# Optimization experiments

Hardware: AMD Instinct MI355X
Metric: run time of the kernel (lower is better)

The kernel has to match this reference:

```python
import jax, jax.numpy as jnp
import numpy as np

CONF_THRES = 0.25
IOU_THRES = 0.45
TOP_K = 1024          # fixed candidate pool per image (jit-friendly padded NMS)
B, N, C = 64, 25200, 16  # yolov5-face: 3*(80^2+40^2+20^2)=25200 anchors, 16 channels
IMG = 640.0


def setup_inputs() -> dict:
    key = jax.random.key(0)
    k1, k2, k3, k4, k5 = jax.random.split(key, 5)
    cxcy = jax.random.uniform(k1, (B, N, 2)) * (IMG - 32.0) + 16.0   # box centers
    wh = jax.random.uniform(k2, (B, N, 2)) * 120.0 + 8.0             # box sizes
    obj = jax.random.uniform(k3, (B, N, 1))                           # objectness
    lm = jax.random.uniform(k4, (B, N, 10)) * IMG                     # 5 landmarks
    cls = jax.random.uniform(k5, (B, N, 1))                           # face class conf
    x = jnp.concatenate([cxcy, wh, obj, lm, cls], axis=-1)            # [B, N, 16]
    return {"x": x}


def _xywh2xyxy(b):
    cx, cy, w, h = b[..., 0], b[..., 1], b[..., 2], b[..., 3]
    return jnp.stack([cx - w * 0.5, cy - h * 0.5, cx + w * 0.5, cy + h * 0.5], axis=-1)


def _pairwise_iou(boxes):
    # boxes: [K, 4] xyxy -> iou: [K, K]
    x1, y1, x2, y2 = boxes[:, 0], boxes[:, 1], boxes[:, 2], boxes[:, 3]
    area = jnp.clip(x2 - x1, 0.0) * jnp.clip(y2 - y1, 0.0)            # [K]
    ix1 = jnp.maximum(x1[:, None], x1[None, :])
    iy1 = jnp.maximum(y1[:, None], y1[None, :])
    ix2 = jnp.minimum(x2[:, None], x2[None, :])
    iy2 = jnp.minimum(y2[:, None], y2[None, :])
    inter = jnp.clip(ix2 - ix1, 0.0) * jnp.clip(iy2 - iy1, 0.0)
    union = area[:, None] + area[None, :] - inter
    return inter / (union + 1e-9)


def _nms_image(pred):
    # pred: [N, 16] = xywh, obj, 10 landmark coords, cls
    score = pred[:, 4] * pred[:, 15]                                   # obj * cls conf
    s = jnp.where(score > CONF_THRES, score, -1.0)                     # conf filter
    top_s, order = jax.lax.top_k(s, TOP_K)                             # sort desc
    valid = top_s > 0.0
    boxes = _xywh2xyxy(pred[order, :4])                                # [K, 4]
    lm = pred[order, 5:15]                                             # [K, 10]
    iou = _pairwise_iou(boxes)                                         # [K, K]
    idx = jnp.arange(TOP_K)

    def body(i, keep):
        # suppress lower-scored boxes overlapping kept box i
        sup = (iou[i] > IOU_THRES) & (idx > i) & keep[i]
        return keep & ~sup

    keep = jax.lax.fori_loop(0, TOP_K, body, valid)
    conf = jnp.where(valid, top_s, 0.0)[:, None]
    cls_id = jnp.zeros((TOP_K, 1), dtype=pred.dtype)                   # single class: face
    dets = jnp.concatenate([boxes, conf, lm, cls_id], axis=-1)         # [K, 16]
    return dets * keep[:, None].astype(dets.dtype)                     # zero suppressed rows


def reference(x):
    # x: [B, N, 16] -> padded detections [B, TOP_K, 16]
    return jax.vmap(_nms_image)(x)
```

## Files before the change

### kernel.cpp

```cpp
#include <hip/hip_runtime.h>
#include <stdint.h>

#define NBOX 25200
#define NCH  16
#define TOPK 1024
#define NTH  1024
#define NBUCK 4096
#define CAP  2048
#define K1_SLICES 16
#define K1_TH 256
#define ROWS_PER_SLICE (NBOX / K1_SLICES)
#define K1_ITERS 7
#define SEGCAP 1600

#define M45 ((double)0.45f + 0x1p-26)

#define OFF_KEYS  4096
#define OFF_BOXES (OFF_KEYS + 64 * K1_SLICES * SEGCAP * 8)
#define OFF_MASKS (OFF_BOXES + 64 * TOPK * 16)

__device__ __forceinline__ unsigned long long make_key(float p, uint32_t r) {
  return ((unsigned long long)__float_as_uint(p) << 32) |
         (unsigned long long)(0xFFFFFFFFu - r);
}

__device__ __forceinline__ uint32_t bucket_of(uint32_t bits) {
  uint32_t bk = (bits - 0x3E800001u) >> 12;
  return bk > (NBUCK - 1u) ? (NBUCK - 1u) : bk;
}

__global__ __launch_bounds__(K1_TH) void score_kernel(const float* __restrict__ x,
                                                      unsigned long long* __restrict__ keys,
                                                      uint32_t* __restrict__ cnts) {
  const int img = blockIdx.x >> 4;
  const int slice = blockIdx.x & (K1_SLICES - 1);
  const int t = threadIdx.x;
  const int lane = t & 63;
  const int wid = t >> 6;
  const float* __restrict__ xb = x + (size_t)img * NBOX * NCH;
  unsigned long long* __restrict__ kl = keys + ((size_t)img * K1_SLICES + slice) * SEGCAP;
  const int row0 = slice * ROWS_PER_SLICE;

  float p[K1_ITERS];
  uint32_t mask = 0;
#pragma unroll
  for (int j = 0; j < K1_ITERS - 1; ++j) {
    const size_t ro = (size_t)(row0 + t + j * K1_TH) * NCH;
    const float v = xb[ro + 4] * xb[ro + 15];
    if (v > 0.25f) mask |= (1u << j);
    p[j] = v;
  }
  {
    const int rr = t + (K1_ITERS - 1) * K1_TH;
    float v = 0.0f;
    if (rr < ROWS_PER_SLICE) {
      const size_t ro = (size_t)(row0 + rr) * NCH;
      v = xb[ro + 4] * xb[ro + 15];
      if (v > 0.25f) mask |= (1u << (K1_ITERS - 1));
    }
    p[K1_ITERS - 1] = v;
  }

  const int cntl = __popc(mask);
  uint32_t inc = (uint32_t)cntl;
#pragma unroll
  for (int off = 1; off < 64; off <<= 1) {
    const uint32_t o = __shfl_up(inc, off);
    if (lane >= off) inc += o;
  }
  const uint32_t wtotal = __shfl(inc, 63);

  __shared__ uint32_t s_wtot[4];
  if (lane == 63) s_wtot[wid] = wtotal;
  __syncthreads();
  uint32_t base = 0;
#pragma unroll
  for (int w = 0; w < 4; ++w) if (w < wid) base += s_wtot[w];

  uint32_t pos = base + (inc - (uint32_t)cntl);
#pragma unroll
  for (int j = 0; j < K1_ITERS; ++j) {
    if ((mask >> j) & 1u) {
      kl[pos] = make_key(p[j], (uint32_t)(row0 + t + j * K1_TH));
      ++pos;
    }
  }
  if (t == K1_TH - 1)
    cnts[img * K1_SLICES + slice] = base + wtotal;
}

__global__ __launch_bounds__(NTH, 1) void select_kernel(const float* __restrict__ x,
                                                        const unsigned long long* __restrict__ keys,
                                                        const uint32_t* __restrict__ cnts,
                                                        float* __restrict__ out,
                                                        float4* __restrict__ boxes) {
  __shared__ uint32_t s_hist[NBUCK];
  __shared__ uint32_t s_pos[NBUCK];
  __shared__ unsigned long long s_sorted[CAP];
  __shared__ unsigned long long s_final[TOPK];
  __shared__ uint32_t s_wsum[16];
  __shared__ uint32_t s_cnt16[K1_SLICES];
  __shared__ int s_cut;

  const int t = threadIdx.x;
  const int b = blockIdx.x;
  const int lane = t & 63;
  const int wid = t >> 6;
  const float* __restrict__ xb = x + (size_t)b * NBOX * NCH;
  const unsigned long long* __restrict__ kb0 = keys + (size_t)b * K1_SLICES * SEGCAP;

#pragma unroll
  for (int j = 0; j < NBUCK / NTH; ++j) s_hist[t + j * NTH] = 0u;
  s_final[t] = 0ull;
  if (t < K1_SLICES) {
    uint32_t c = cnts[b * K1_SLICES + t];
    s_cnt16[t] = (c > SEGCAP) ? SEGCAP : c;
  }
  if (t == 0) s_cut = 0;
  __syncthreads();
#pragma unroll
  for (int s = 0; s < K1_SLICES; ++s) {
    const int cs_ = (int)s_cnt16[s];
    const unsigned long long* seg = kb0 + (size_t)s * SEGCAP;
    for (int j = t; j < cs_; j += NTH)
      atomicAdd(&s_hist[bucket_of((uint32_t)(seg[j] >> 32))], 1u);
  }
  __syncthreads();

  const uint32_t h0 = s_hist[4 * t], h1 = s_hist[4 * t + 1];
  const uint32_t h2 = s_hist[4 * t + 2], h3 = s_hist[4 * t + 3];
  const uint32_t qs = h0 + h1 + h2 + h3;
  uint32_t v = qs;
#pragma unroll
  for (int off = 1; off < 64; off <<= 1) {
    const uint32_t o = __shfl_down(v, off);
    if (lane + off < 64) v += o;
  }
  if (lane == 0) s_wsum[wid] = v;
  __syncthreads();
  uint32_t tail = 0;
#pragma unroll
  for (int w = 0; w < 16; ++w) if (w > wid) tail += s_wsum[w];
  const uint32_t after = (v - qs) + tail;
  const uint32_t e3 = after, e2 = after + h3, e1 = e2 + h2, e0 = e1 + h1;
  s_pos[4 * t] = e0; s_pos[4 * t + 1] = e1;
  s_pos[4 * t + 2] = e2; s_pos[4 * t + 3] = e3;
  int cand = -1;
  if (e3 + h3 >= TOPK) cand = 4 * t + 3;
  else if (e2 + h2 >= TOPK) cand = 4 * t + 2;
  else if (e1 + h1 >= TOPK) cand = 4 * t + 1;
  else if (e0 + h0 >= TOPK) cand = 4 * t;
  int wmax = cand;
#pragma unroll
  for (int off = 32; off > 0; off >>= 1) {
    const int o = __shfl_down(wmax, off);
    if (o > wmax) wmax = o;
  }
  if (lane == 0 && wmax >= 0) atomicMax(&s_cut, wmax);
  __syncthreads();
  const int cut = s_cut;
  int M = (int)(s_pos[cut] + s_hist[cut]);
  if (M > CAP) M = CAP;
  __syncthreads();

#pragma unroll
  for (int s = 0; s < K1_SLICES; ++s) {
    const int cs_ = (int)s_cnt16[s];
    const unsigned long long* seg = kb0 + (size_t)s * SEGCAP;
    for (int j = t; j < cs_; j += NTH) {
      const unsigned long long key = seg[j];
      const uint32_t bk = bucket_of((uint32_t)(key >> 32));
      if ((int)bk >= cut) {
        const uint32_t pos = atomicAdd(&s_pos[bk], 1u);
        if (pos < CAP) s_sorted[pos] = key;
      }
    }
  }
  __syncthreads();

  for (int p = t; p < M; p += NTH) {
    const unsigned long long key = s_sorted[p];
    const uint32_t bk = bucket_of((uint32_t)(key >> 32));
    int end = (int)s_pos[bk]; if (end > M) end = M;
    int start = end - (int)s_hist[bk]; if (start < 0) start = 0;
    int lr = 0;
    for (int q = start; q < end; ++q) lr += (int)(s_sorted[q] > key);
    const int fp = start + lr;
    if (fp < TOPK) s_final[fp] = key;
  }
  __syncthreads();

  const unsigned long long mykey = s_final[t];
  const uint32_t sbits = (uint32_t)(mykey >> 32);
  const int src = (int)(0xFFFFFFFFu - (uint32_t)(mykey & 0xFFFFFFFFull));
  const bool valid = (sbits != 0u);
  const float conf = valid ? __uint_as_float(sbits) : 0.0f;

  float x1 = 0.f, y1 = 0.f, x2 = 0.f, y2 = 0.f;
  float lm0=0.f,lm1=0.f,lm2=0.f,lm3=0.f,lm4=0.f,lm5=0.f,lm6=0.f,lm7=0.f,lm8=0.f,lm9=0.f;
  if (valid) {
    const float4* rp = (const float4*)(xb + (size_t)src * NCH);
    const float4 q0 = rp[0], q1 = rp[1], q2 = rp[2], q3 = rp[3];
    x1 = q0.x - q0.z * 0.5f;
    y1 = q0.y - q0.w * 0.5f;
    x2 = q0.x + q0.z * 0.5f;
    y2 = q0.y + q0.w * 0.5f;
    lm0 = q1.y; lm1 = q1.z; lm2 = q1.w;
    lm3 = q2.x; lm4 = q2.y; lm5 = q2.z; lm6 = q2.w;
    lm7 = q3.x; lm8 = q3.y; lm9 = q3.z;
  }
  boxes[(size_t)b * TOPK + t] = make_float4(x1, y1, x2, y2);
  float4* op = (float4*)(out + ((size_t)b * TOPK + (size_t)t) * NCH);
  op[0] = make_float4(x1, y1, x2, y2);
  op[1] = make_float4(conf, lm0, lm1, lm2);
  op[2] = make_float4(lm3, lm4, lm5, lm6);
  op[3] = make_float4(lm7, lm8, lm9, 0.0f);
}

__global__ __launch_bounds__(256) void mask_kernel(const float4* __restrict__ boxes,
                                                   unsigned long long* __restrict__ masks) {
  const int img = blockIdx.x / 40;
  const int s = blockIdx.x % 40;
  int rt, wg;
  if (s < 4)        { rt = s;                wg = 0; }
  else if (s < 12)  { rt = 4 + ((s - 4) >> 1);  wg = (s - 4) & 1; }
  else if (s < 24)  { rt = 8 + (s - 12) / 3;    wg = (s - 12) % 3; }
  else              { rt = 12 + ((s - 24) >> 2); wg = (s - 24) & 3; }

  const int t = threadIdx.x;
  const int lane = t & 63;
  const int jw = wg * 4 + (t >> 6);

  __shared__ float4 s_rbox[64];
  __shared__ float s_rarea[64];
  if (t < 64) {
    const float4 rb = boxes[(size_t)img * TOPK + rt * 64 + t];
    s_rbox[t] = rb;
    s_rarea[t] = fmaxf(rb.z - rb.x, 0.f) * fmaxf(rb.w - rb.y, 0.f);
  }
  __syncthreads();
  if (jw > rt) return;

  const float4 cb = boxes[(size_t)img * TOPK + jw * 64 + lane];
  const float ca = fmaxf(cb.z - cb.x, 0.f) * fmaxf(cb.w - cb.y, 0.f);

  unsigned long long myword = 0ull;
  for (int rl = 0; rl < 64; ++rl) {
    const float4 rb = s_rbox[rl];
    const float ra = s_rarea[rl];
    const float iw = fmaxf(fminf(cb.z, rb.z) - fmaxf(cb.x, rb.x), 0.f);
    const float ih = fmaxf(fminf(cb.w, rb.w) - fmaxf(cb.y, rb.y), 0.f);
    const float inter = iw * ih;
    const float den = ((ca + ra) - inter) + 1e-9f;
    const bool sup = (double)inter > M45 * (double)den;
    unsigned long long bal = __ballot(sup);
    if (jw == rt) bal &= ((1ull << rl) - 1ull);
    if (lane == rl) myword = bal;
  }
  masks[((size_t)img * 16 + jw) * TOPK + rt * 64 + lane] = myword;
}

__global__ __launch_bounds__(NTH, 1) void greedy_kernel(const unsigned long long* __restrict__ masks,
                                                        float* __restrict__ out) {
  __shared__ unsigned long long s_alive[16];
  const int t = threadIdx.x;
  const int b = blockIdx.x;
  const int lane = t & 63;
  const int wid = t >> 6;

  const unsigned long long diag = masks[((size_t)b * 16 + wid) * TOPK + t];

  bool keep = true;
  unsigned long long acc = 0ull;

  for (int tile = 0; tile < 16; ++tile) {
    unsigned long long mw = 0ull;
    if (wid > tile) mw = masks[((size_t)b * 16 + tile) * TOPK + t];

    if (wid == tile) {
      if (acc) keep = false;
      unsigned long long vm = __ballot(diag != 0ull);
      while (vm) {
        const int vv = __ffsll((long long)vm) - 1;
        vm &= vm - 1ull;
        const unsigned long long alive = __ballot(keep);
        if (lane == vv && (alive & diag)) keep = false;
      }
      const unsigned long long fin = __ballot(keep);
      if (lane == 0) s_alive[tile] = fin;
    }
    __syncthreads();
    if (wid > tile) acc |= mw & s_alive[tile];
  }

  if (!keep) {
    float4* op = (float4*)(out + ((size_t)b * TOPK + (size_t)t) * NCH);
    const float4 z = make_float4(0.f, 0.f, 0.f, 0.f);
    op[0] = z; op[1] = z; op[2] = z; op[3] = z;
  }
}

extern "C" void kernel_launch(void* const* d_in, const int* in_sizes, int n_in,
                              void* d_out, int out_size, void* d_ws, size_t ws_size,
                              hipStream_t stream) {
  const float* x = (const float*)d_in[0];
  float* out = (float*)d_out;
  uint32_t* cnts = (uint32_t*)d_ws;
  unsigned long long* keys = (unsigned long long*)((char*)d_ws + OFF_KEYS);
  float4* boxes = (float4*)((char*)d_ws + OFF_BOXES);
  unsigned long long* masks = (unsigned long long*)((char*)d_ws + OFF_MASKS);

  score_kernel<<<dim3(64 * K1_SLICES), dim3(K1_TH), 0, stream>>>(x, keys, cnts);
  select_kernel<<<dim3(64), dim3(NTH), 0, stream>>>(x, keys, cnts, out, boxes);
  mask_kernel<<<dim3(64 * 40), dim3(256), 0, stream>>>(boxes, masks);
  greedy_kernel<<<dim3(64), dim3(NTH), 0, stream>>>(masks, out);
}
```

Baseline: 206.6 us.

## Fuse greedy NMS into mask kernel via last-block-arrives counter

Merges the greedy suppression kernel into the IoU mask kernel. Each block increments a per-image completion counter, and the last of the 40 blocks for an image runs the greedy scan with 256 threads, each handling 4 rows. This removes one kernel launch and lets greedy work for early-finishing images overlap mask work for other images. In exchange, the greedy pass runs with a quarter of the threads and adds threadfence and atomic overhead.

Measured after the change: 407.6 us. 97.3% more time.

```diff
diff --git a/kernel.cpp b/kernel.cpp
--- a/kernel.cpp
+++ b/kernel.cpp
@@ -18,6 +18,7 @@
 #define OFF_KEYS  4096
 #define OFF_BOXES (OFF_KEYS + 64 * K1_SLICES * SEGCAP * 8)
 #define OFF_MASKS (OFF_BOXES + 64 * TOPK * 16)
+#define OFF_DONE  (OFF_MASKS + 64 * 16 * TOPK * 8)
 
 __device__ __forceinline__ unsigned long long make_key(float p, uint32_t r) {
   return ((unsigned long long)__float_as_uint(p) << 32) |
@@ -93,7 +94,8 @@
                                                         const unsigned long long* __restrict__ keys,
                                                         const uint32_t* __restrict__ cnts,
                                                         float* __restrict__ out,
-                                                        float4* __restrict__ boxes) {
+                                                        float4* __restrict__ boxes,
+                                                        uint32_t* __restrict__ done) {
   __shared__ uint32_t s_hist[NBUCK];
   __shared__ uint32_t s_pos[NBUCK];
   __shared__ unsigned long long s_sorted[CAP];
@@ -116,7 +118,7 @@
     uint32_t c = cnts[b * K1_SLICES + t];
     s_cnt16[t] = (c > SEGCAP) ? SEGCAP : c;
   }
-  if (t == 0) s_cut = 0;
+  if (t == 0) { s_cut = 0; done[b] = 0u; }
   __syncthreads();
 #pragma unroll
   for (int s = 0; s < K1_SLICES; ++s) {
@@ -217,8 +219,10 @@
   op[3] = make_float4(lm7, lm8, lm9, 0.0f);
 }
 
-__global__ __launch_bounds__(256) void mask_kernel(const float4* __restrict__ boxes,
-                                                   unsigned long long* __restrict__ masks) {
+__global__ __launch_bounds__(256) void mask_greedy_kernel(const float4* __restrict__ boxes,
+                                                          unsigned long long* __restrict__ masks,
+                                                          uint32_t* __restrict__ done,
+                                                          float* __restrict__ out) {
   const int img = blockIdx.x / 40;
   const int s = blockIdx.x % 40;
   int rt, wg;
@@ -229,74 +233,93 @@
 
   const int t = threadIdx.x;
   const int lane = t & 63;
-  const int jw = wg * 4 + (t >> 6);
+  const int wid = t >> 6;
+  const int jw = wg * 4 + wid;
 
   __shared__ float4 s_rbox[64];
   __shared__ float s_rarea[64];
+  __shared__ uint32_t s_arriv;
   if (t < 64) {
     const float4 rb = boxes[(size_t)img * TOPK + rt * 64 + t];
     s_rbox[t] = rb;
     s_rarea[t] = fmaxf(rb.z - rb.x, 0.f) * fmaxf(rb.w - rb.y, 0.f);
   }
   __syncthreads();
-  if (jw > rt) return;
-
-  const float4 cb = boxes[(size_t)img * TOPK + jw * 64 + lane];
-  const float ca = fmaxf(cb.z - cb.x, 0.f) * fmaxf(cb.w - cb.y, 0.f);
-
-  unsigned long long myword = 0ull;
-  for (int rl = 0; rl < 64; ++rl) {
-    const float4 rb = s_rbox[rl];
-    const float ra = s_rarea[rl];
-    const float iw = fmaxf(fminf(cb.z, rb.z) - fmaxf(cb.x, rb.x), 0.f);
-    const float ih = fmaxf(fminf(cb.w, rb.w) - fmaxf(cb.y, rb.y), 0.f);
-    const float inter = iw * ih;
-    const float den = ((ca + ra) - inter) + 1e-9f;
-    const bool sup = (double)inter > M45 * (double)den;
-    unsigned long long bal = __ballot(sup);
-    if (jw == rt) bal &= ((1ull << rl) - 1ull);
-    if (lane == rl) myword = bal;
-  }
-  masks[((size_t)img * 16 + jw) * TOPK + rt * 64 + lane] = myword;
-}
-
-__global__ __launch_bounds__(NTH, 1) void greedy_kernel(const unsigned long long* __restrict__ masks,
-                                                        float* __restrict__ out) {
+
+  if (jw <= rt) {
+    const float4 cb = boxes[(size_t)img * TOPK + jw * 64 + lane];
+    const float ca = fmaxf(cb.z - cb.x, 0.f) * fmaxf(cb.w - cb.y, 0.f);
+    unsigned long long myword = 0ull;
+    for (int rl = 0; rl < 64; ++rl) {
+      const float4 rb = s_rbox[rl];
+      const float ra = s_rarea[rl];
+      const float iw = fmaxf(fminf(cb.z, rb.z) - fmaxf(cb.x, rb.x), 0.f);
+      const float ih = fmaxf(fminf(cb.w, rb.w) - fmaxf(cb.y, rb.y), 0.f);
+      const float inter = iw * ih;
+      const float den = ((ca + ra) - inter) + 1e-9f;
+      const bool sup = (double)inter > M45 * (double)den;
+      unsigned long long bal = __ballot(sup);
+      if (jw == rt) bal &= ((1ull << rl) - 1ull);
+      if (lane == rl) myword = bal;
+    }
+    masks[((size_t)img * 16 + jw) * TOPK + rt * 64 + lane] = myword;
+  }
+
+  __threadfence();
+  __syncthreads();
+  if (t == 0) s_arriv = atomicAdd(&done[img], 1u);
+  __syncthreads();
+  if (s_arriv != 39u) return;
+  __threadfence();
+
+  const unsigned long long* __restrict__ mb = masks + (size_t)img * 16 * TOPK;
   __shared__ unsigned long long s_alive[16];
-  const int t = threadIdx.x;
-  const int b = blockIdx.x;
-  const int lane = t & 63;
-  const int wid = t >> 6;
-
-  const unsigned long long diag = masks[((size_t)b * 16 + wid) * TOPK + t];
-
-  bool keep = true;
-  unsigned long long acc = 0ull;
-
-  for (int tile = 0; tile < 16; ++tile) {
-    unsigned long long mw = 0ull;
-    if (wid > tile) mw = masks[((size_t)b * 16 + tile) * TOPK + t];
-
-    if (wid == tile) {
-      if (acc) keep = false;
-      unsigned long long vm = __ballot(diag != 0ull);
+  unsigned long long diag[4], acc4[4];
+  bool keep4[4];
+#pragma unroll
+  for (int k = 0; k < 4; ++k) {
+    const int tile = 4 * k + wid;
+    diag[k] = mb[(size_t)tile * TOPK + (k * 256 + t)];
+    acc4[k] = 0ull;
+    keep4[k] = true;
+  }
+
+  for (int T = 0; T < 16; ++T) {
+    unsigned long long mw[4];
+#pragma unroll
+    for (int k = 0; k < 4; ++k)
+      mw[k] = (4 * k + wid > T) ? mb[(size_t)T * TOPK + (k * 256 + t)] : 0ull;
+
+    if ((T & 3) == wid) {
+      const int k = T >> 2;
+      bool kp = keep4[k];
+      if (acc4[k]) kp = false;
+      const unsigned long long dg = diag[k];
+      unsigned long long vm = __ballot(dg != 0ull);
       while (vm) {
         const int vv = __ffsll((long long)vm) - 1;
         vm &= vm - 1ull;
-        const unsigned long long alive = __ballot(keep);
-        if (lane == vv && (alive & diag)) keep = false;
+        const unsigned long long alive = __ballot(kp);
+        if (lane == vv && (alive & dg)) kp = false;
       }
-      const unsigned long long fin = __ballot(keep);
-      if (lane == 0) s_alive[tile] = fin;
+      keep4[k] = kp;
+      const unsigned long long fin = __ballot(kp);
+      if (lane == 0) s_alive[T] = fin;
     }
     __syncthreads();
-    if (wid > tile) acc |= mw & s_alive[tile];
-  }
-
-  if (!keep) {
-    float4* op = (float4*)(out + ((size_t)b * TOPK + (size_t)t) * NCH);
-    const float4 z = make_float4(0.f, 0.f, 0.f, 0.f);
-    op[0] = z; op[1] = z; op[2] = z; op[3] = z;
+    const unsigned long long am = s_alive[T];
+#pragma unroll
+    for (int k = 0; k < 4; ++k)
+      if (4 * k + wid > T) acc4[k] |= mw[k] & am;
+  }
+
+#pragma unroll
+  for (int k = 0; k < 4; ++k) {
+    if (!keep4[k]) {
+      float4* op = (float4*)(out + ((size_t)img * TOPK + (size_t)(k * 256 + t)) * NCH);
+      const float4 z = make_float4(0.f, 0.f, 0.f, 0.f);
+      op[0] = z; op[1] = z; op[2] = z; op[3] = z;
+    }
   }
 }
 
@@ -309,9 +332,9 @@
   unsigned long long* keys = (unsigned long long*)((char*)d_ws + OFF_KEYS);
   float4* boxes = (float4*)((char*)d_ws + OFF_BOXES);
   unsigned long long* masks = (unsigned long long*)((char*)d_ws + OFF_MASKS);
+  uint32_t* done = (uint32_t*)((char*)d_ws + OFF_DONE);
 
   score_kernel<<<dim3(64 * K1_SLICES), dim3(K1_TH), 0, stream>>>(x, keys, cnts);
-  select_kernel<<<dim3(64), dim3(NTH), 0, stream>>>(x, keys, cnts, out, boxes);
-  mask_kernel<<<dim3(64 * 40), dim3(256), 0, stream>>>(boxes, masks);
-  greedy_kernel<<<dim3(64), dim3(NTH), 0, stream>>>(masks, out);
-}
+  select_kernel<<<dim3(64), dim3(NTH), 0, stream>>>(x, keys, cnts, out, boxes, done);
+  mask_greedy_kernel<<<dim3(64 * 40), dim3(256), 0, stream>>>(boxes, masks, done, out);
+}
```
